# Kernel optimization log

Hardware: AMD Instinct MI355X
Metric: run time of the kernel (lower is better)

## Reference

```python
import jax, jax.numpy as jnp
import numpy as np

N_NODES = 50000
EPS_NORM = 1e-12
EPS_ENT = 1e-8

def _l2norm(x):
    # torch.nn.functional.normalize: x / clamp(||x||, min=1e-12)
    n = jnp.sqrt(jnp.sum(x * x, axis=-1, keepdims=True))
    return x / jnp.maximum(n, EPS_NORM)

def _layer(hidden, src, dst, edge_type, multi_emb, proto_emb):
    # hidden: [N,H]; multi_emb: [R,P,H]; proto_emb: [P,H]
    inp_j = hidden[src]                          # [E,H] gather
    rel_basis = multi_emb[edge_type]             # [E,P,H] gather
    sims = jnp.einsum('eh,ph->ep', _l2norm(inp_j), _l2norm(proto_emb))  # cosine sim [E,P]
    proto_proba = jax.nn.softmax(sims, axis=1)   # [E,P]
    msg = jnp.einsum('ep,eph->eh', proto_proba, rel_basis)              # [E,H]
    ent = -jnp.sum(proto_proba * jnp.log(proto_proba + EPS_ENT), axis=1)  # [E]
    logits = -ent
    # scatter_softmax over destination index
    seg_max = jax.ops.segment_max(logits, dst, num_segments=N_NODES)
    ex = jnp.exp(logits - seg_max[dst])
    denom = jax.ops.segment_sum(ex, dst, num_segments=N_NODES)
    attn = ex / denom[dst]                       # [E]
    out = jax.ops.segment_sum(attn[:, None] * msg, dst, num_segments=N_NODES)  # [N,H]
    return out

def setup_inputs() -> dict:
    key = jax.random.key(0)
    ks = jax.random.split(key, 6)
    E = 800000
    H, R, P, L = 128, 18, 18, 3  # num_layers=4 -> 3 NBFCluttr layers
    edge_index = jax.random.randint(ks[0], (2, E), 0, N_NODES, dtype=jnp.int64) if jax.config.read('jax_enable_x64') else jax.random.randint(ks[0], (2, E), 0, N_NODES, dtype=jnp.int32)
    edge_type = jax.random.randint(ks[1], (E,), 0, R, dtype=edge_index.dtype)
    tail_indices = jax.random.randint(ks[2], (1024,), 0, N_NODES, dtype=edge_index.dtype)
    multi_embeddings = jax.random.uniform(ks[3], (L, R, P, H), dtype=jnp.float32)
    proto_embeddings = jax.random.uniform(ks[4], (L, P, H), dtype=jnp.float32)
    source_embedding = jax.random.uniform(ks[5], (H,), dtype=jnp.float32)
    return {"edge_index": edge_index, "edge_type": edge_type, "tail_indices": tail_indices,
            "multi_embeddings": multi_embeddings, "proto_embeddings": proto_embeddings,
            "source_embedding": source_embedding}

def reference(edge_index, edge_type, tail_indices, multi_embeddings, proto_embeddings, source_embedding):
    src, dst = edge_index[0], edge_index[1]
    H = source_embedding.shape[0]
    # boundary condition: source node gets source_embedding, rest zero
    hidden = jnp.zeros((N_NODES, H), dtype=source_embedding.dtype).at[0].set(source_embedding)
    L = multi_embeddings.shape[0]
    for l in range(L):  # small fixed loop over structurally distinct layers
        hidden = _layer(hidden, src, dst, edge_type, multi_embeddings[l], proto_embeddings[l])
    # apply_classifier, eval_mode=True, use_mlp_classifier=False -> cosine sims to last layer prototypes
    out_emb = hidden[tail_indices]               # [B,H]
    sims = jnp.einsum('nh,ph->np', _l2norm(out_emb), _l2norm(proto_embeddings[-1]))
    return sims  # gumbel_softmax_sample with eval_mode=True returns logits unchanged
```

## Files before the change

kernel.cpp:

```cpp
#include <hip/hip_runtime.h>
#include <hip/hip_bf16.h>


#define N_NODES 50000
#define H 128
#define P 18
#define RP 324
#define KPAD 352
#define K0PAD 64
#define ELLW 64

typedef _Float16 half8 __attribute__((ext_vector_type(8)));
typedef float floatx4 __attribute__((ext_vector_type(4)));

__global__ __launch_bounds__(256) void zero_u32_kernel(unsigned* p, int n) {
  int i = blockIdx.x * 256 + threadIdx.x;
  if (i < n) p[i] = 0u;
}

__global__ __launch_bounds__(256) void ell_kernel(const int* __restrict__ src,
                                                  const int* __restrict__ dst,
                                                  const int* __restrict__ etype,
                                                  unsigned* __restrict__ cur,
                                                  unsigned* __restrict__ ep, int E) {
  int i = blockIdx.x * 256 + threadIdx.x;
  if (i < E) {
    int d = dst[i];
    unsigned pos = atomicAdd(&cur[d], 1u);
    if (pos < ELLW)
      ep[(size_t)d * ELLW + pos] = (unsigned)src[i] | ((unsigned)etype[i] << 20);
  }
}

__global__ __launch_bounds__(64) void proto_norm_kernel(const float* __restrict__ proto,
                                                        float* __restrict__ pN) {
  int row = blockIdx.x, l = threadIdx.x;
  float a = proto[row * H + l], b = proto[row * H + 64 + l];
  float ss = a * a + b * b;
  for (int m = 32; m > 0; m >>= 1) ss += __shfl_xor(ss, m, 64);
  float inv = 1.f / fmaxf(sqrtf(ss), 1e-12f);
  pN[row * H + l] = a * inv;
  pN[row * H + 64 + l] = b * inv;
}

__global__ __launch_bounds__(256) void bprep_kernel(const float* __restrict__ multi,
                                                    _Float16* __restrict__ Btg) {
  int idx = blockIdx.x * 256 + threadIdx.x;
  if (idx >= 2 * H * KPAD) return;
  int l = idx / (H * KPAD), rem = idx - l * (H * KPAD);
  int h = rem / KPAD, k = rem - h * KPAD;
  const float* B = multi + (size_t)(l + 1) * RP * H;
  Btg[idx] = (k < RP) ? (_Float16)B[k * H + h] : (_Float16)0.f;
}

__global__ __launch_bounds__(64) void q0_kernel(const float* __restrict__ semb,
                                                const float* __restrict__ pN,
                                                float* __restrict__ q0r) {
  int l = threadIdx.x;
  float s0 = semb[l], s1 = semb[l + 64];
  float ss = s0 * s0 + s1 * s1;
  float dot[P];
#pragma unroll
  for (int p = 0; p < P; p++) dot[p] = s0 * pN[p * H + l] + s1 * pN[p * H + 64 + l];
  for (int m = 1; m <= 32; m <<= 1) {
    ss += __shfl_xor(ss, m, 64);
#pragma unroll
    for (int p = 0; p < P; p++) dot[p] += __shfl_xor(dot[p], m, 64);
  }
  float inv = 1.f / fmaxf(sqrtf(ss), 1e-12f);
  float sum = 0.f;
#pragma unroll
  for (int p = 0; p < P; p++) {
    dot[p] = __expf(dot[p] * inv - 1.f);
    sum += dot[p];
  }
  float isum = 1.f / sum, ent = 0.f;
#pragma unroll
  for (int p = 0; p < P; p++) {
    dot[p] *= isum;
    ent -= dot[p] * __logf(dot[p] + 1e-8f);
  }
  float w = __expf(-ent);
  if (l < P) q0r[l] = w * dot[l];
}

__global__ __launch_bounds__(256) void bl0_prep_kernel(const float* __restrict__ B,
                                                       const float* __restrict__ q0r,
                                                       _Float16* __restrict__ Bt) {
  int idx = blockIdx.x * 256 + threadIdx.x;
  if (idx >= H * K0PAD) return;
  int h = idx >> 6, k = idx & 63;
  float pr = 1.f / 18.f, ent = 0.f;
#pragma unroll
  for (int p = 0; p < P; p++) ent -= pr * __logf(pr + 1e-8f);
  float qc = __expf(-ent) * pr;
  float v = 0.f;
  if (k < P) {
#pragma unroll
    for (int p = 0; p < P; p++) v += qc * B[(k * P + p) * H + h];
  } else if (k < 2 * P) {
    int r = k - P;
#pragma unroll
    for (int p = 0; p < P; p++) v += (q0r[p] - qc) * B[(r * P + p) * H + h];
  }
  Bt[h * K0PAD + k] = (_Float16)v;
}

__global__ __launch_bounds__(256) void hist_kernel(const unsigned* __restrict__ ep,
                                                   const unsigned* __restrict__ cur,
                                                   _Float16* __restrict__ M, int n) {
  int wave = threadIdx.x >> 6, lane = threadIdx.x & 63;
  int nd = blockIdx.x * 4 + wave;
  if (nd >= n) return;
  int cnt = (int)cur[nd];
  if (cnt > ELLW) cnt = ELLW;
  bool a = lane < cnt;
  unsigned pk = a ? ep[(size_t)nd * ELLW + lane] : 0xFFFFFFFFu;
  int r = (int)(pk >> 20);
  unsigned long long zm = __ballot(a && (pk & 0xFFFFFu) == 0u);
  float creg = 0.f, creg0 = 0.f;
#pragma unroll
  for (int rr = 0; rr < P; rr++) {
    unsigned long long m = __ballot(a && (r == rr));
    if (lane == rr) {
      creg = (float)__popcll(m);
      creg0 = (float)__popcll(m & zm);
    }
  }
  int slx = (lane >= P && lane < 2 * P) ? lane - P : 0;
  float v0 = __shfl(creg0, slx, 64);
  float val = (lane < P) ? creg : ((lane < 2 * P) ? v0 : 0.f);
  M[(size_t)nd * K0PAD + lane] = (_Float16)val;
}

__global__ __launch_bounds__(256) void scatter_kernel(const unsigned* __restrict__ ep,
                                                      const unsigned* __restrict__ cur,
                                                      const float* __restrict__ q,
                                                      const int* __restrict__ tl,
                                                      _Float16* __restrict__ M, int n) {
  __shared__ float sl[4][3 * RP];
  int wave = threadIdx.x >> 6, lane = threadIdx.x & 63;
  int t = blockIdx.x * 4 + wave;
  float* s0 = sl[wave];
  for (int i = lane; i < 3 * RP; i += 64) s0[i] = 0.f;
  int sub = lane / 18;
  int j = lane - sub * 18;
  bool act = (sub < 3) && (t < n);
  int cnt = 0;
  size_t b = 0;
  if (t < n) {
    int nd = tl ? tl[t] : t;
    b = (size_t)nd * ELLW;
    cnt = (int)cur[nd];
    if (cnt > ELLW) cnt = ELLW;
  }
  float* ms = s0 + (sub < 3 ? sub : 0) * RP;
  for (int it = 0; it < cnt; it += 9) {
    bool a0 = act && (it + sub < cnt);
    bool a1 = act && (it + 3 + sub < cnt);
    bool a2 = act && (it + 6 + sub < cnt);
    unsigned pk0 = 0, pk1 = 0, pk2 = 0;
    if (a0) pk0 = ep[b + it + sub];
    if (a1) pk1 = ep[b + it + 3 + sub];
    if (a2) pk2 = ep[b + it + 6 + sub];
    float q0 = 0.f, q1 = 0.f, q2 = 0.f;
    if (a0) q0 = q[(size_t)(pk0 & 0xFFFFFu) * P + j];
    if (a1) q1 = q[(size_t)(pk1 & 0xFFFFFu) * P + j];
    if (a2) q2 = q[(size_t)(pk2 & 0xFFFFFu) * P + j];
    if (a0) ms[(pk0 >> 20) * P + j] += q0;
    if (a1) ms[(pk1 >> 20) * P + j] += q1;
    if (a2) ms[(pk2 >> 20) * P + j] += q2;
  }
  if (t < n) {
    for (int k = lane; k < RP; k += 64)
      M[(size_t)t * KPAD + k] = (_Float16)(s0[k] + s0[RP + k] + s0[2 * RP + k]);
    for (int k = RP + lane; k < KPAD; k += 64) M[(size_t)t * KPAD + k] = (_Float16)0.f;
  }
}

template <int MODE>
__global__ __launch_bounds__(256) void gemm_kernel(const _Float16* __restrict__ M,
                                                   const _Float16* __restrict__ Bt,
                                                   const float* __restrict__ pN,
                                                   float* __restrict__ q_out, int n,
                                                   int kpad) {
  __shared__ float smem_f[64 * 132];
  _Float16* As = (_Float16*)smem_f;
  _Float16* Bs = (_Float16*)(smem_f + 1024);
  int tid = threadIdx.x;
  int wave = tid >> 6, lane = tid & 63;
  int m15 = lane & 15, quad = lane >> 4;
  int n0 = blockIdx.x * 64;
  floatx4 acc[4][2] = {};

  __shared__ float pns[4 * P * 36];
  for (int i = tid; i < 4 * P * 32; i += 256) {
    int s = i / (P * 32), r = i - s * (P * 32);
    int p = r >> 5, kk = r & 31;
    pns[s * (P * 36) + p * 36 + kk] = pN[p * H + s * 32 + kk];
  }

  for (int kt = 0; kt < (kpad >> 5); kt++) {
    int k0 = kt * 32;
    __syncthreads();
    {
      int row = tid >> 2, kc = (tid & 3) * 8;
      int gr = n0 + row;
      half8 v = {};
      if (gr < n) v = *(const half8*)(M + (size_t)gr * kpad + k0 + kc);
      *(half8*)(As + row * 32 + kc) = v;
    }
    {
      int col = tid >> 1, kc = (tid & 1) * 16;
      const _Float16* srcp = Bt + (size_t)col * kpad + k0 + kc;
      *(half8*)(Bs + col * 32 + kc) = *(const half8*)srcp;
      *(half8*)(Bs + col * 32 + kc + 8) = *(const half8*)(srcp + 8);
    }
    __syncthreads();
    half8 bfrag0 = *(const half8*)(Bs + (wave * 32 + m15) * 32 + quad * 8);
    half8 bfrag1 = *(const half8*)(Bs + (wave * 32 + 16 + m15) * 32 + quad * 8);
#pragma unroll
    for (int mt = 0; mt < 4; mt++) {
      half8 afrag = *(const half8*)(As + (mt * 16 + m15) * 32 + quad * 8);
      acc[mt][0] = __builtin_amdgcn_mfma_f32_16x16x32_f16(afrag, bfrag0, acc[mt][0], 0, 0, 0);
      acc[mt][1] = __builtin_amdgcn_mfma_f32_16x16x32_f16(afrag, bfrag1, acc[mt][1], 0, 0, 0);
    }
  }
  __syncthreads();
#pragma unroll
  for (int mt = 0; mt < 4; mt++)
#pragma unroll
    for (int c = 0; c < 2; c++)
#pragma unroll
      for (int reg = 0; reg < 4; reg++)
        smem_f[(mt * 16 + quad * 4 + reg) * 132 + wave * 32 + c * 16 + m15] = acc[mt][c][reg];
  __syncthreads();
  int node = tid >> 2, sub = tid & 3;
  int gnode = n0 + node;
  const float* trow = smem_f + node * 132 + sub * 32;
  const float* ps = pns + sub * (P * 36);
  float ss = 0.f;
  float dot[P];
#pragma unroll
  for (int p = 0; p < P; p++) dot[p] = 0.f;
#pragma unroll
  for (int k4 = 0; k4 < 8; k4++) {
    float4 y = *(const float4*)(trow + k4 * 4);
    ss += y.x * y.x + y.y * y.y + y.z * y.z + y.w * y.w;
#pragma unroll
    for (int p = 0; p < P; p++) {
      float4 b = *(const float4*)(ps + p * 36 + k4 * 4);
      dot[p] += y.x * b.x + y.y * b.y + y.z * b.z + y.w * b.w;
    }
  }
  for (int m = 1; m <= 2; m <<= 1) {
    ss += __shfl_xor(ss, m, 64);
#pragma unroll
    for (int p = 0; p < P; p++) dot[p] += __shfl_xor(dot[p], m, 64);
  }
  if (gnode < n) {
    float inv = 1.f / fmaxf(sqrtf(ss), 1e-12f);
    if (MODE == 1) {
      for (int p = sub; p < P; p += 4) q_out[(size_t)gnode * P + p] = dot[p] * inv;
    } else {
      float sum = 0.f;
#pragma unroll
      for (int p = 0; p < P; p++) {
        dot[p] = __expf(dot[p] * inv - 1.f);
        sum += dot[p];
      }
      float isum = 1.f / sum, ent = 0.f;
#pragma unroll
      for (int p = 0; p < P; p++) {
        dot[p] *= isum;
        ent -= dot[p] * __logf(dot[p] + 1e-8f);
      }
      float w = __expf(-ent);
      for (int p = sub; p < P; p += 4) q_out[(size_t)gnode * P + p] = w * dot[p];
    }
  }
}

extern "C" void kernel_launch(void* const* d_in, const int* in_sizes, int n_in,
                              void* d_out, int out_size, void* d_ws, size_t ws_size,
                              hipStream_t stream) {
  const int* eidx = (const int*)d_in[0];
  int E = in_sizes[0] / 2;
  const int* src = eidx;
  const int* dst = eidx + E;
  const int* etype = (const int*)d_in[1];
  const int* tails = (const int*)d_in[2];
  int T = in_sizes[2];
  const float* multi = (const float*)d_in[3];
  const float* proto = (const float*)d_in[4];
  const float* semb = (const float*)d_in[5];
  float* out = (float*)d_out;

  char* w = (char*)d_ws;
  auto alloc = [&](size_t bytes) {
    char* p = w;
    w += (bytes + 255) & ~(size_t)255;
    return p;
  };
  float* q = (float*)alloc((size_t)N_NODES * P * 4);
  float* q0r = (float*)alloc((size_t)P * 4);
  float* pNs = (float*)alloc((size_t)3 * P * H * 4);
  _Float16* Mg = (_Float16*)alloc((size_t)N_NODES * KPAD * 2);
  _Float16* Btg = (_Float16*)alloc((size_t)2 * H * KPAD * 2);
  _Float16* Btl0 = (_Float16*)alloc((size_t)H * K0PAD * 2);
  unsigned* cur = (unsigned*)alloc((size_t)N_NODES * 4);
  unsigned* ep = (unsigned*)alloc((size_t)N_NODES * ELLW * 4);

  int nb = (N_NODES + 255) / 256;
  int eb = (E + 255) / 256;

  zero_u32_kernel<<<nb, 256, 0, stream>>>(cur, N_NODES);
  ell_kernel<<<eb, 256, 0, stream>>>(src, dst, etype, cur, ep, E);

  proto_norm_kernel<<<3 * P, 64, 0, stream>>>(proto, pNs);
  bprep_kernel<<<(2 * H * KPAD + 255) / 256, 256, 0, stream>>>(multi, Btg);
  q0_kernel<<<1, 64, 0, stream>>>(semb, pNs, q0r);
  bl0_prep_kernel<<<(H * K0PAD + 255) / 256, 256, 0, stream>>>(multi, q0r, Btl0);

  hist_kernel<<<(N_NODES + 3) / 4, 256, 0, stream>>>(ep, cur, Mg, N_NODES);
  gemm_kernel<0><<<(N_NODES + 63) / 64, 256, 0, stream>>>(Mg, Btl0, pNs + (size_t)1 * P * H, q,
                                                          N_NODES, K0PAD);

  scatter_kernel<<<(N_NODES + 3) / 4, 256, 0, stream>>>(ep, cur, q, nullptr, Mg, N_NODES);
  gemm_kernel<0><<<(N_NODES + 63) / 64, 256, 0, stream>>>(Mg, Btg, pNs + (size_t)2 * P * H, q,
                                                          N_NODES, KPAD);

  scatter_kernel<<<(T + 3) / 4, 256, 0, stream>>>(ep, cur, q, tails, Mg, T);
  gemm_kernel<1><<<(T + 63) / 64, 256, 0, stream>>>(Mg, Btg + (size_t)H * KPAD,
                                                    pNs + (size_t)2 * P * H, out, T, KPAD);
}
```

Measured before the change: 252.3 us.

## Partition ELL build by destination range and merge small prep kernels

The ELL construction kernel now runs NPART times as many blocks. Each block keeps only edges whose destination falls in its node partition, which localises the atomic counter traffic and ELL writes to a smaller region per partition. The dst array is read eight times in exchange. Separately, four tiny setup kernels are merged into two: prototype normalisation and the q0 computation share one launch, and the two B-prep kernels share another, to cut launch overhead. The merged bprep computes Btl0 from q0r, which is written by the preceding protoq0 kernel. Same-stream ordering keeps that dependency safe.

```diff
diff --git a/kernel.cpp b/kernel.cpp
--- a/kernel.cpp
+++ b/kernel.cpp
@@ -9,6 +9,8 @@
 #define KPAD 352
 #define K0PAD 64
 #define ELLW 64
+#define NPART 8
+#define NODES_PER_PART 6250
 
 typedef _Float16 half8 __attribute__((ext_vector_type(8)));
 typedef float floatx4 __attribute__((ext_vector_type(4)));
@@ -23,45 +25,42 @@
                                                   const int* __restrict__ etype,
                                                   unsigned* __restrict__ cur,
                                                   unsigned* __restrict__ ep, int E) {
-  int i = blockIdx.x * 256 + threadIdx.x;
-  if (i < E) {
-    int d = dst[i];
-    unsigned pos = atomicAdd(&cur[d], 1u);
-    if (pos < ELLW)
-      ep[(size_t)d * ELLW + pos] = (unsigned)src[i] | ((unsigned)etype[i] << 20);
-  }
-}
-
-__global__ __launch_bounds__(64) void proto_norm_kernel(const float* __restrict__ proto,
-                                                        float* __restrict__ pN) {
+  int part = blockIdx.x & (NPART - 1);
+  int i = (blockIdx.x >> 3) * 256 + threadIdx.x;
+  if (i >= E) return;
+  int d = dst[i];
+  int lo = part * NODES_PER_PART;
+  if (d < lo || d >= lo + NODES_PER_PART) return;
+  unsigned pos = atomicAdd(&cur[d], 1u);
+  if (pos < ELLW)
+    ep[(size_t)d * ELLW + pos] = (unsigned)src[i] | ((unsigned)etype[i] << 20);
+}
+
+__global__ __launch_bounds__(64) void protoq0_kernel(const float* __restrict__ proto,
+                                                     const float* __restrict__ semb,
+                                                     float* __restrict__ pN,
+                                                     float* __restrict__ q0r) {
   int row = blockIdx.x, l = threadIdx.x;
-  float a = proto[row * H + l], b = proto[row * H + 64 + l];
-  float ss = a * a + b * b;
-  for (int m = 32; m > 0; m >>= 1) ss += __shfl_xor(ss, m, 64);
-  float inv = 1.f / fmaxf(sqrtf(ss), 1e-12f);
-  pN[row * H + l] = a * inv;
-  pN[row * H + 64 + l] = b * inv;
-}
-
-__global__ __launch_bounds__(256) void bprep_kernel(const float* __restrict__ multi,
-                                                    _Float16* __restrict__ Btg) {
-  int idx = blockIdx.x * 256 + threadIdx.x;
-  if (idx >= 2 * H * KPAD) return;
-  int l = idx / (H * KPAD), rem = idx - l * (H * KPAD);
-  int h = rem / KPAD, k = rem - h * KPAD;
-  const float* B = multi + (size_t)(l + 1) * RP * H;
-  Btg[idx] = (k < RP) ? (_Float16)B[k * H + h] : (_Float16)0.f;
-}
-
-__global__ __launch_bounds__(64) void q0_kernel(const float* __restrict__ semb,
-                                                const float* __restrict__ pN,
-                                                float* __restrict__ q0r) {
-  int l = threadIdx.x;
+  if (row < 54) {
+    float a = proto[row * H + l], b = proto[row * H + 64 + l];
+    float ss = a * a + b * b;
+    for (int m = 32; m > 0; m >>= 1) ss += __shfl_xor(ss, m, 64);
+    float inv = 1.f / fmaxf(sqrtf(ss), 1e-12f);
+    pN[row * H + l] = a * inv;
+    pN[row * H + 64 + l] = b * inv;
+    return;
+  }
   float s0 = semb[l], s1 = semb[l + 64];
   float ss = s0 * s0 + s1 * s1;
   float dot[P];
 #pragma unroll
-  for (int p = 0; p < P; p++) dot[p] = s0 * pN[p * H + l] + s1 * pN[p * H + 64 + l];
+  for (int p = 0; p < P; p++) {
+    float a = proto[p * H + l], b = proto[p * H + 64 + l];
+    float rn = a * a + b * b;
+    for (int m = 32; m > 0; m >>= 1) rn += __shfl_xor(rn, m, 64);
+    float rinv = 1.f / fmaxf(sqrtf(rn), 1e-12f);
+    dot[p] = (s0 * a + s1 * b) * rinv;
+  }
   for (int m = 1; m <= 32; m <<= 1) {
     ss += __shfl_xor(ss, m, 64);
 #pragma unroll
@@ -84,12 +83,21 @@
   if (l < P) q0r[l] = w * dot[l];
 }
 
-__global__ __launch_bounds__(256) void bl0_prep_kernel(const float* __restrict__ B,
-                                                       const float* __restrict__ q0r,
-                                                       _Float16* __restrict__ Bt) {
+__global__ __launch_bounds__(256) void bprep_kernel(const float* __restrict__ multi,
+                                                    const float* __restrict__ q0r,
+                                                    _Float16* __restrict__ Btg,
+                                                    _Float16* __restrict__ Btl0) {
   int idx = blockIdx.x * 256 + threadIdx.x;
-  if (idx >= H * K0PAD) return;
-  int h = idx >> 6, k = idx & 63;
+  if (idx < 2 * H * KPAD) {
+    int l = idx / (H * KPAD), rem = idx - l * (H * KPAD);
+    int h = rem / KPAD, k = rem - h * KPAD;
+    const float* B = multi + (size_t)(l + 1) * RP * H;
+    Btg[idx] = (k < RP) ? (_Float16)B[k * H + h] : (_Float16)0.f;
+    return;
+  }
+  int idx2 = idx - 2 * H * KPAD;
+  if (idx2 >= H * K0PAD) return;
+  int h = idx2 >> 6, k = idx2 & 63;
   float pr = 1.f / 18.f, ent = 0.f;
 #pragma unroll
   for (int p = 0; p < P; p++) ent -= pr * __logf(pr + 1e-8f);
@@ -97,13 +105,13 @@
   float v = 0.f;
   if (k < P) {
 #pragma unroll
-    for (int p = 0; p < P; p++) v += qc * B[(k * P + p) * H + h];
+    for (int p = 0; p < P; p++) v += qc * multi[(k * P + p) * H + h];
   } else if (k < 2 * P) {
     int r = k - P;
 #pragma unroll
-    for (int p = 0; p < P; p++) v += (q0r[p] - qc) * B[(r * P + p) * H + h];
-  }
-  Bt[h * K0PAD + k] = (_Float16)v;
+    for (int p = 0; p < P; p++) v += (q0r[p] - qc) * multi[(r * P + p) * H + h];
+  }
+  Btl0[h * K0PAD + k] = (_Float16)v;
 }
 
 __global__ __launch_bounds__(256) void hist_kernel(const unsigned* __restrict__ ep,
@@ -315,12 +323,11 @@
   int eb = (E + 255) / 256;
 
   zero_u32_kernel<<<nb, 256, 0, stream>>>(cur, N_NODES);
-  ell_kernel<<<eb, 256, 0, stream>>>(src, dst, etype, cur, ep, E);
-
-  proto_norm_kernel<<<3 * P, 64, 0, stream>>>(proto, pNs);
-  bprep_kernel<<<(2 * H * KPAD + 255) / 256, 256, 0, stream>>>(multi, Btg);
-  q0_kernel<<<1, 64, 0, stream>>>(semb, pNs, q0r);
-  bl0_prep_kernel<<<(H * K0PAD + 255) / 256, 256, 0, stream>>>(multi, q0r, Btl0);
+  ell_kernel<<<eb * NPART, 256, 0, stream>>>(src, dst, etype, cur, ep, E);
+
+  protoq0_kernel<<<55, 64, 0, stream>>>(proto, semb, pNs, q0r);
+  bprep_kernel<<<(2 * H * KPAD + H * K0PAD + 255) / 256, 256, 0, stream>>>(multi, q0r, Btg,
+                                                                           Btl0);
 
   hist_kernel<<<(N_NODES + 3) / 4, 256, 0, stream>>>(ep, cur, Mg, N_NODES);
   gemm_kernel<0><<<(N_NODES + 63) / 64, 256, 0, stream>>>(Mg, Btl0, pNs + (size_t)1 * P * H, q,
```

Measured after the change: 241.8 us. -4.1%, faster.
